# Performance work log

Measured on AMD Instinct MI355X. Metric: run time of the kernel, lower is better.

## Reference

```python
import jax, jax.numpy as jnp
import numpy as np


def _pn_layer(x, W):
    # x: [B, d]; W: [N, d+1, d+1]. z = [x, 1]; out[b, n] = z_b^T W_n z_b
    z = jnp.concatenate([x, jnp.ones((x.shape[0], 1), dtype=x.dtype)], axis=1)  # [B, d+1]
    zW = jnp.einsum('bi,nij->bnj', z, W)      # [B, N, d+1]
    return jnp.einsum('bnj,bj->bn', zW, z)    # [B, N]


def setup_inputs() -> dict:
    key = jax.random.key(0)
    k_x, k1, k2, k3, kw, kb = jax.random.split(key, 6)
    B, D = 2048, 256
    return {
        'x': jax.random.normal(k_x, (B, D), dtype=jnp.float32),
        'W1': jax.random.normal(k1, (256, D + 1, D + 1), dtype=jnp.float32),
        'W2': jax.random.normal(k2, (256, 257, 257), dtype=jnp.float32),
        'W3': jax.random.normal(k3, (256, 257, 257), dtype=jnp.float32),
        'w_out': jax.random.normal(kw, (1, 256), dtype=jnp.float32),
        'b_out': jax.random.normal(kb, (1,), dtype=jnp.float32),
    }


def reference(x, W1, W2, W3, w_out, b_out):
    h = _pn_layer(x, W1)   # [B, 256]
    h = _pn_layer(h, W2)   # [B, 256]
    h = _pn_layer(h, W3)   # [B, 256]
    return h @ w_out.T + b_out  # [B, 1]
```

## Files before the change

### kernel.cpp

```cpp
#include <hip/hip_runtime.h>
#include <hip/hip_bf16.h>

typedef __attribute__((ext_vector_type(8))) short short8;
typedef __attribute__((ext_vector_type(4))) float f32x4;

#define DDIM 256
#define WROW 257
#define WSTRIDE 66049
#define WT3_N 36864

__device__ __forceinline__ unsigned short f2bf(float f) {
    unsigned int u = __float_as_uint(f);
    u += 0x7fff + ((u >> 16) & 1);
    return (unsigned short)(u >> 16);
}
__device__ __forceinline__ float bf2f(unsigned short s) {
    return __uint_as_float(((unsigned int)s) << 16);
}


__global__ __launch_bounds__(256) void conv_w3_kernel(
    const float* __restrict__ Wf, unsigned short* __restrict__ Wt3,
    float* __restrict__ Vt, float* __restrict__ Dv)
{
    __shared__ float tKJ[64][65];
    __shared__ float tJK[64][65];
    const int TJ[10] = {0,1,1,2,2,2,3,3,3,3};
    const int TK[10] = {0,0,1,0,1,2,0,1,2,3};
    const int tid = threadIdx.x;
    const int n   = blockIdx.y;
    const int tj  = TJ[blockIdx.x];
    const int tk  = TK[blockIdx.x];
    const float* Wn = Wf + (size_t)n * WSTRIDE;
    if (blockIdx.x == 0) {
        int j = tid;
        Vt[n * 256 + j] = Wn[(size_t)j * WROW + 256] + Wn[65792 + j];
        if (j == 0) Dv[n] = Wn[66048];
    }
    #pragma unroll
    for (int it = 0; it < 4; ++it) {
        int idx = it * 256 + tid;
        int r   = idx >> 4;
        int c4  = (idx & 15) * 4;
        float4 vKJ = *reinterpret_cast<const float4*>(&Wn[(size_t)(tk * 64 + r) * WROW + tj * 64 + c4]);
        float4 vJK = *reinterpret_cast<const float4*>(&Wn[(size_t)(tj * 64 + r) * WROW + tk * 64 + c4]);
        tKJ[r][c4 + 0] = vKJ.x; tKJ[r][c4 + 1] = vKJ.y; tKJ[r][c4 + 2] = vKJ.z; tKJ[r][c4 + 3] = vKJ.w;
        tJK[r][c4 + 0] = vJK.x; tJK[r][c4 + 1] = vJK.y; tJK[r][c4 + 2] = vJK.z; tJK[r][c4 + 3] = vJK.w;
    }
    __syncthreads();
    unsigned short* out = Wt3 + (size_t)n * WT3_N;
    #pragma unroll
    for (int it = 0; it < 8; ++it) {
        int jl = it * 8 + (tid >> 5);
        int k2 = (tid & 31) * 2;
        int jg = tj * 64 + jl;
        int kg = tk * 64 + k2;
        int jt = jg >> 5;
        int kk = kg >> 5;
        if (kk <= jt) {
            float sc = (kk == jt) ? 0.5f : 1.0f;
            float v0 = sc * (tKJ[k2][jl]     + tJK[jl][k2]);
            float v1 = sc * (tKJ[k2 + 1][jl] + tJK[jl][k2 + 1]);
            unsigned int u = (unsigned)f2bf(v0) | ((unsigned)f2bf(v1) << 16);
            int half = (jg >> 4) & 1;
            int r15l = jg & 15;
            int qwl  = (kg >> 3) & 3;
            int kr   = kg & 7;
            size_t sidx = (size_t)(jt * (jt + 1) / 2 + kk) * 1024 + half * 512
                        + (qwl * 16 + r15l) * 8 + kr;
            *reinterpret_cast<unsigned int*>(out + sidx) = u;
        }
    }
}

__device__ __forceinline__ void xe_gather3(const unsigned short* T, unsigned short* Xe2,
                                           int bx, int tid) {
    const int lane = tid & 63, g = tid >> 6, qw = (tid >> 4) & 3, r15 = tid & 15;
    #pragma unroll
    for (int it = 0; it < 16; ++it) {
        int c  = g * 16 + it;
        int h  = c >> 5;
        int jt = (c >> 2) & 7;
        int m  = c & 3;
        int rbase = h * 64 + m * 16 + qw * 4;
        int jA = jt * 32 + r15;
        unsigned int u0 = T[(rbase + 0) * 256 + jA];
        unsigned int u1 = T[(rbase + 1) * 256 + jA];
        unsigned int u2 = T[(rbase + 2) * 256 + jA];
        unsigned int u3 = T[(rbase + 3) * 256 + jA];
        unsigned int v0 = T[(rbase + 0) * 256 + jA + 16];
        unsigned int v1 = T[(rbase + 1) * 256 + jA + 16];
        unsigned int v2 = T[(rbase + 2) * 256 + jA + 16];
        unsigned int v3 = T[(rbase + 3) * 256 + jA + 16];
        uint4 w = make_uint4(u0 | (u1 << 16), u2 | (u3 << 16),
                             v0 | (v1 << 16), v2 | (v3 << 16));
        *reinterpret_cast<uint4*>(Xe2 + ((size_t)(bx * 2 + h) * 16384 + jt * 2048 + m * 512 + lane * 8)) = w;
    }
}

__global__ __launch_bounds__(256) void conv_x_rm_kernel(
    const float* __restrict__ X, unsigned short* __restrict__ Xbf, unsigned short* __restrict__ Xe2)
{
    __shared__ __align__(16) unsigned short T[128 * 256];
    const int tid = threadIdx.x;
    const int b0 = blockIdx.x * 128;
    const float4* Xv = reinterpret_cast<const float4*>(X + (size_t)b0 * 256);
    uint2* Xo = reinterpret_cast<uint2*>(Xbf + (size_t)b0 * 256);
    #pragma unroll
    for (int it = 0; it < 32; ++it) {
        int idx4 = it * 256 + tid;
        float4 v = Xv[idx4];
        uint2 p;
        p.x = (unsigned)f2bf(v.x) | ((unsigned)f2bf(v.y) << 16);
        p.y = (unsigned)f2bf(v.z) | ((unsigned)f2bf(v.w) << 16);
        *reinterpret_cast<uint2*>(&T[idx4 * 4]) = p;
        Xo[idx4] = p;
    }
    __syncthreads();
    xe_gather3(T, Xe2, blockIdx.x, tid);
}

__global__ __launch_bounds__(256) void conv_x_tr_kernel(
    const unsigned short* __restrict__ Hsrc, unsigned short* __restrict__ Xbf,
    unsigned short* __restrict__ Xe2)
{
    __shared__ __align__(16) unsigned short T[128 * 256];
    const int tid = threadIdx.x;
    const int b0 = blockIdx.x * 128;
    #pragma unroll
    for (int it = 0; it < 64; ++it) {
        int lin = it * 256 + tid;
        int k = lin >> 6, bp = lin & 63;
        unsigned int v = *reinterpret_cast<const unsigned int*>(Hsrc + (size_t)k * 2048 + b0 + bp * 2);
        T[(bp * 2) * 256 + k]     = (unsigned short)(v & 0xffff);
        T[(bp * 2 + 1) * 256 + k] = (unsigned short)(v >> 16);
    }
    __syncthreads();
    uint4* Xo = reinterpret_cast<uint4*>(Xbf + (size_t)b0 * 256);
    #pragma unroll
    for (int it = 0; it < 16; ++it) {
        int idx8 = it * 256 + tid;
        Xo[idx8] = *reinterpret_cast<uint4*>(&T[idx8 * 8]);
    }
    xe_gather3(T, Xe2, blockIdx.x, tid);
}

__global__ __launch_bounds__(256, 2) void pn10_kernel(
    const unsigned short* __restrict__ Xbf,
    const unsigned short* __restrict__ Xe2,
    const unsigned short* __restrict__ Wt3,
    const float* __restrict__ Vt,
    const float* __restrict__ Dv,
    unsigned short* __restrict__ Ht)
{
    __shared__ __align__(16) char Xl[32768];

    const int tid  = threadIdx.x;
    const int lane = tid & 63;
    const int wv   = tid >> 6;
    const int qw   = lane >> 4;
    const int r15  = lane & 15;

    const int fid = blockIdx.y * 32 + blockIdx.x;
    const int bt  = (fid >> 3) & 31;
    const int ng  = (fid & 7) + ((fid >> 8) << 3);
    const int n   = ng * 4 + wv;
    const int b0  = bt * 64;

    {
        const uint4* xs = reinterpret_cast<const uint4*>(Xbf + (size_t)b0 * 256);
        #pragma unroll
        for (int c = 0; c < 8; ++c) {
            int idx = c * 256 + tid;
            uint4 v = xs[idx];
            int L = idx * 16;
            int d = L ^ (((L >> 9) & 7) << 4);
            *reinterpret_cast<uint4*>(&Xl[d]) = v;
        }
    }

    const unsigned short* wp = Wt3 + (size_t)n * WT3_N + (size_t)lane * 8;
    const float* vn = Vt + n * 256;
    const unsigned short* xe = Xe2 + (size_t)bt * 16384 + (size_t)lane * 8;

    short8 bA0 = *reinterpret_cast<const short8*>(wp);
    short8 bB0 = *reinterpret_cast<const short8*>(wp + 512);
    short8 bA1 = *reinterpret_cast<const short8*>(wp + 1024);
    short8 bB1 = *reinterpret_cast<const short8*>(wp + 1024 + 512);
    short8 bA2 = *reinterpret_cast<const short8*>(wp + 2048);
    short8 bB2 = *reinterpret_cast<const short8*>(wp + 2048 + 512);
    short8 bA3 = *reinterpret_cast<const short8*>(wp + 3072);
    short8 bB3 = *reinterpret_cast<const short8*>(wp + 3072 + 512);

    short8 e0 = *reinterpret_cast<const short8*>(xe);
    short8 e1 = *reinterpret_cast<const short8*>(xe + 512);
    short8 e2 = *reinterpret_cast<const short8*>(xe + 1024);
    short8 e3 = *reinterpret_cast<const short8*>(xe + 1536);
    float vA = vn[r15], vB = vn[16 + r15];

    float ps[4][4];
    f32x4 a0[4], a1[4];
    #pragma unroll
    for (int m = 0; m < 4; ++m) {
        a0[m] = f32x4{0.f, 0.f, 0.f, 0.f};
        a1[m] = f32x4{0.f, 0.f, 0.f, 0.f};
        #pragma unroll
        for (int r = 0; r < 4; ++r) ps[m][r] = 0.f;
    }

    int jt = 0, kk = 0;
    int slab_pf = 4;

    __syncthreads();

    auto body = [&](short8& bA, short8& bB) {
        #pragma unroll
        for (int m = 0; m < 4; ++m) {
            const int row = m * 16 + r15;
            const int byte = (row * 512 + kk * 64 + qw * 16) ^ ((row & 7) << 4);
            short8 a = *reinterpret_cast<const short8*>(&Xl[byte]);
            a0[m] = __builtin_amdgcn_mfma_f32_16x16x32_bf16(a, bA, a0[m], 0, 0, 0);
            a1[m] = __builtin_amdgcn_mfma_f32_16x16x32_bf16(a, bB, a1[m], 0, 0, 0);
        }
        if (kk == jt) {
            #pragma unroll
            for (int r = 0; r < 4; ++r) {
                ps[0][r] += (a0[0][r] + vA) * bf2f((unsigned short)e0[r]) + (a1[0][r] + vB) * bf2f((unsigned short)e0[4 + r]);
                ps[1][r] += (a0[1][r] + vA) * bf2f((unsigned short)e1[r]) + (a1[1][r] + vB) * bf2f((unsigned short)e1[4 + r]);
                ps[2][r] += (a0[2][r] + vA) * bf2f((unsigned short)e2[r]) + (a1[2][r] + vB) * bf2f((unsigned short)e2[4 + r]);
                ps[3][r] += (a0[3][r] + vA) * bf2f((unsigned short)e3[r]) + (a1[3][r] + vB) * bf2f((unsigned short)e3[4 + r]);
            }
            #pragma unroll
            for (int m = 0; m < 4; ++m) {
                a0[m] = f32x4{0.f, 0.f, 0.f, 0.f};
                a1[m] = f32x4{0.f, 0.f, 0.f, 0.f};
            }
            jt += 1; kk = 0;
            const int jc = (jt < 8) ? jt : 7;
            e0 = *reinterpret_cast<const short8*>(xe + jc * 2048);
            e1 = *reinterpret_cast<const short8*>(xe + jc * 2048 + 512);
            e2 = *reinterpret_cast<const short8*>(xe + jc * 2048 + 1024);
            e3 = *reinterpret_cast<const short8*>(xe + jc * 2048 + 1536);
            vA = vn[jc * 32 + r15];
            vB = vn[jc * 32 + 16 + r15];
        } else {
            kk += 1;
        }
        const int sc = (slab_pf <= 35) ? slab_pf : 35;
        const unsigned short* pf = wp + (size_t)sc * 1024;
        bA = *reinterpret_cast<const short8*>(pf);
        bB = *reinterpret_cast<const short8*>(pf + 512);
        slab_pf += 1;
    };

    #pragma unroll 1
    for (int i = 0; i < 9; ++i) {
        body(bA0, bB0);
        body(bA1, bB1);
        body(bA2, bB2);
        body(bA3, bB3);
    }

    #pragma unroll
    for (int off = 1; off <= 8; off <<= 1)
        #pragma unroll
        for (int m = 0; m < 4; ++m)
            #pragma unroll
            for (int r = 0; r < 4; ++r) ps[m][r] += __shfl_xor(ps[m][r], off, 64);

    if (r15 == 0) {
        const float dn = Dv[n];
        #pragma unroll
        for (int m = 0; m < 4; ++m)
            #pragma unroll
            for (int r = 0; r < 4; ++r)
                Ht[(size_t)n * 2048 + b0 + m * 16 + qw * 4 + r] = f2bf(ps[m][r] + dn);
    }
}

__global__ __launch_bounds__(256) void out_tr_kernel(
    const unsigned short* __restrict__ H3, const float* __restrict__ w_out,
    const float* __restrict__ b_out, float* __restrict__ out)
{
    __shared__ float red2[256];
    const int tid = threadIdx.x;
    const int b = blockIdx.x * 128 + (tid & 127);
    const int half = tid >> 7;
    float s = 0.f;
    #pragma unroll 8
    for (int k = 0; k < 128; ++k) {
        int nn = half * 128 + k;
        s += bf2f(H3[(size_t)nn * 2048 + b]) * w_out[nn];
    }
    red2[tid] = s;
    __syncthreads();
    if (tid < 128) out[b] = red2[tid] + red2[tid + 128] + b_out[0];
}


__global__ __launch_bounds__(256, 2) void pn_layer_kernel(
    const float* __restrict__ X, const float* __restrict__ W, float* __restrict__ H)
{
    __shared__ __align__(16) char Xl[64 * 256 * 2];
    __shared__ __align__(16) char Wl[2][256 * 32 * 2];
    const int tid  = threadIdx.x;
    const int lane = tid & 63;
    const int wv   = tid >> 6;
    const int qw   = lane >> 4;
    const int r15  = lane & 15;
    const int n  = blockIdx.y;
    const int b0 = blockIdx.x * 64;
    const float* Wn = W + (size_t)n * WSTRIDE;
    {
        const float4* Xv = reinterpret_cast<const float4*>(X + (size_t)b0 * DDIM);
        #pragma unroll
        for (int it = 0; it < 16; ++it) {
            int idx4 = tid + it * 256;
            int r = idx4 >> 6, c4 = idx4 & 63;
            float4 v = Xv[r * 64 + c4];
            uint2 p;
            p.x = (unsigned)f2bf(v.x) | ((unsigned)f2bf(v.y) << 16);
            p.y = (unsigned)f2bf(v.z) | ((unsigned)f2bf(v.w) << 16);
            int byte = (r * 512 + c4 * 8) ^ ((r & 7) << 4);
            *reinterpret_cast<uint2*>(&Xl[byte]) = p;
        }
    }
    f32x4 acc[4][4];
    #pragma unroll
    for (int nf = 0; nf < 4; ++nf) {
        int j = wv * 64 + nf * 16 + r15;
        float vj = Wn[(size_t)j * WROW + 256] + Wn[65792 + j];
        #pragma unroll
        for (int m = 0; m < 4; ++m) acc[m][nf] = f32x4{vj, vj, vj, vj};
    }
    auto stageW = [&](int buf, int kk) {
        const int k0 = kk * 32;
        const int j  = tid;
        float t[32];
        #pragma unroll
        for (int k = 0; k < 32; ++k) t[k] = Wn[(size_t)(k0 + k) * WROW + j];
        char* Wb = Wl[buf];
        #pragma unroll
        for (int g = 0; g < 4; ++g) {
            unsigned int p0 = (unsigned)f2bf(t[g*8+0]) | ((unsigned)f2bf(t[g*8+1]) << 16);
            unsigned int p1 = (unsigned)f2bf(t[g*8+2]) | ((unsigned)f2bf(t[g*8+3]) << 16);
            unsigned int p2 = (unsigned)f2bf(t[g*8+4]) | ((unsigned)f2bf(t[g*8+5]) << 16);
            unsigned int p3 = (unsigned)f2bf(t[g*8+6]) | ((unsigned)f2bf(t[g*8+7]) << 16);
            int byte = (j * 64 + g * 16) ^ ((j & 7) << 4);
            *reinterpret_cast<uint4*>(&Wb[byte]) = make_uint4(p0, p1, p2, p3);
        }
    };
    auto computeK = [&](int buf, int kk) {
        char* Wb = Wl[buf];
        short8 a[4], bbf[4];
        #pragma unroll
        for (int m = 0; m < 4; ++m) {
            int row = m * 16 + r15;
            int byte = (row * 512 + kk * 64 + qw * 16) ^ ((row & 7) << 4);
            a[m] = *reinterpret_cast<short8*>(&Xl[byte]);
        }
        #pragma unroll
        for (int nf = 0; nf < 4; ++nf) {
            int j = wv * 64 + nf * 16 + r15;
            int byte = (j * 64 + qw * 16) ^ ((j & 7) << 4);
            bbf[nf] = *reinterpret_cast<short8*>(&Wb[byte]);
        }
        #pragma unroll
        for (int m = 0; m < 4; ++m)
            #pragma unroll
            for (int nf = 0; nf < 4; ++nf)
                acc[m][nf] = __builtin_amdgcn_mfma_f32_16x16x32_bf16(a[m], bbf[nf], acc[m][nf], 0, 0, 0);
    };
    stageW(0, 0);
    int cur = 0;
    #pragma unroll
    for (int kk = 0; kk < 8; ++kk) {
        __syncthreads();
        if (kk < 7) stageW(cur ^ 1, kk + 1);
        computeK(cur, kk);
        cur ^= 1;
    }
    float ps[16];
    #pragma unroll
    for (int i = 0; i < 16; ++i) ps[i] = 0.f;
    #pragma unroll
    for (int m = 0; m < 4; ++m)
        #pragma unroll
        for (int nf = 0; nf < 4; ++nf) {
            int j = wv * 64 + nf * 16 + r15;
            #pragma unroll
            for (int r = 0; r < 4; ++r) {
                int brow = m * 16 + qw * 4 + r;
                int byte = (brow * 512 + j * 2) ^ ((brow & 7) << 4);
                float xv = bf2f(*reinterpret_cast<unsigned short*>(&Xl[byte]));
                ps[m * 4 + r] += acc[m][nf][r] * xv;
            }
        }
    #pragma unroll
    for (int off = 1; off <= 8; off <<= 1)
        #pragma unroll
        for (int i = 0; i < 16; ++i) ps[i] += __shfl_xor(ps[i], off, 64);
    __syncthreads();
    float* red = reinterpret_cast<float*>(Wl);
    if (r15 == 0) {
        #pragma unroll
        for (int m = 0; m < 4; ++m)
            #pragma unroll
            for (int r = 0; r < 4; ++r)
                red[wv * 64 + m * 16 + qw * 4 + r] = ps[m * 4 + r];
    }
    __syncthreads();
    if (tid < 64) {
        float s = red[tid] + red[64 + tid] + red[128 + tid] + red[192 + tid] + Wn[66048];
        H[(size_t)(b0 + tid) * DDIM + n] = s;
    }
}

__global__ __launch_bounds__(256) void out_kernel(
    const float* __restrict__ H, const float* __restrict__ w_out,
    const float* __restrict__ b_out, float* __restrict__ out)
{
    int b = blockIdx.x * 4 + (threadIdx.x >> 6);
    int lane = threadIdx.x & 63;
    const float* h = H + (size_t)b * 256;
    float s = 0.f;
    #pragma unroll
    for (int c = 0; c < 4; ++c) s += h[lane + c * 64] * w_out[lane + c * 64];
    #pragma unroll
    for (int off = 1; off < 64; off <<= 1) s += __shfl_xor(s, off, 64);
    if (lane == 0) out[b] = s + b_out[0];
}

extern "C" void kernel_launch(void* const* d_in, const int* in_sizes, int n_in,
                              void* d_out, int out_size, void* d_ws, size_t ws_size,
                              hipStream_t stream) {
    const float* x    = (const float*)d_in[0];
    const float* W1   = (const float*)d_in[1];
    const float* W2   = (const float*)d_in[2];
    const float* W3   = (const float*)d_in[3];
    const float* wout = (const float*)d_in[4];
    const float* bout = (const float*)d_in[5];
    float* out = (float*)d_out;

    const size_t WT3_BYTES = (size_t)256 * WT3_N * 2;
    const size_t XB_BYTES  = (size_t)2048 * 256 * 2;
    const size_t XE2_BYTES = (size_t)32 * 16384 * 2;
    const size_t VT_BYTES  = 256 * 256 * 4;
    const size_t DV_BYTES  = 1024;
    const size_t HT_BYTES  = (size_t)256 * 2048 * 2;
    const size_t need = WT3_BYTES + XB_BYTES + XE2_BYTES + VT_BYTES + DV_BYTES + HT_BYTES;

    dim3 blk(256, 1, 1);

    if (ws_size >= need) {
        char* p = (char*)d_ws;
        unsigned short* Wt3 = (unsigned short*)p;              p += WT3_BYTES;
        unsigned short* Xbf = (unsigned short*)p;              p += XB_BYTES;
        unsigned short* Xe2 = (unsigned short*)p;              p += XE2_BYTES;
        float*          Vt  = (float*)p;                       p += VT_BYTES;
        float*          Dv  = (float*)p;                       p += DV_BYTES;
        unsigned short* Ht  = (unsigned short*)p;

        const float* Ws[3] = {W1, W2, W3};

        dim3 wgrid(10, 256), lgrid(32, 64), xgrid(16);
        for (int L = 0; L < 3; ++L) {
            if (L == 0) conv_x_rm_kernel<<<xgrid, blk, 0, stream>>>(x, Xbf, Xe2);
            else        conv_x_tr_kernel<<<xgrid, blk, 0, stream>>>(Ht, Xbf, Xe2);
            conv_w3_kernel<<<wgrid, blk, 0, stream>>>(Ws[L], Wt3, Vt, Dv);
            pn10_kernel<<<lgrid, blk, 0, stream>>>(Xbf, Xe2, Wt3, Vt, Dv, Ht);
        }
        out_tr_kernel<<<xgrid, blk, 0, stream>>>(Ht, wout, bout, out);
    } else {
        float* h1 = (float*)d_ws;
        float* h2 = h1 + 2048 * 256;
        dim3 grid(32, 256);
        pn_layer_kernel<<<grid, blk, 0, stream>>>(x,  W1, h1);
        pn_layer_kernel<<<grid, blk, 0, stream>>>(h1, W2, h2);
        pn_layer_kernel<<<grid, blk, 0, stream>>>(h2, W3, h1);
        out_kernel<<<512, blk, 0, stream>>>(h1, wout, bout, out);
    }
}
```

Measured before the change: 270.8 us.

## Vectorize packed-weight store in conv kernel and raise pn10 occupancy bound

The weight conversion kernel now assigns whole 16x32 packed chunks to each wavefront, so every lane writes a single 16-byte uint4 instead of scattered 4-byte stores, and only the chunks in the lower-triangular region are enumerated. This reduces the number of store instructions and improves write coalescing. The main pn10 kernel's launch bound is raised from 2 to 3 blocks per SM, which caps register use to allow more resident blocks and risks register spills.

```diff
diff --git a/kernel.cpp b/kernel.cpp
--- a/kernel.cpp
+++ b/kernel.cpp
@@ -48,28 +48,33 @@
         tJK[r][c4 + 0] = vJK.x; tJK[r][c4 + 1] = vJK.y; tJK[r][c4 + 2] = vJK.z; tJK[r][c4 + 3] = vJK.w;
     }
     __syncthreads();
+    const int wv = tid >> 6, lane = tid & 63;
     unsigned short* out = Wt3 + (size_t)n * WT3_N;
-    #pragma unroll
-    for (int it = 0; it < 8; ++it) {
-        int jl = it * 8 + (tid >> 5);
-        int k2 = (tid & 31) * 2;
-        int jg = tj * 64 + jl;
-        int kg = tk * 64 + k2;
-        int jt = jg >> 5;
-        int kk = kg >> 5;
-        if (kk <= jt) {
-            float sc = (kk == jt) ? 0.5f : 1.0f;
-            float v0 = sc * (tKJ[k2][jl]     + tJK[jl][k2]);
-            float v1 = sc * (tKJ[k2 + 1][jl] + tJK[jl][k2 + 1]);
-            unsigned int u = (unsigned)f2bf(v0) | ((unsigned)f2bf(v1) << 16);
-            int half = (jg >> 4) & 1;
-            int r15l = jg & 15;
-            int qwl  = (kg >> 3) & 3;
-            int kr   = kg & 7;
-            size_t sidx = (size_t)(jt * (jt + 1) / 2 + kk) * 1024 + half * 512
-                        + (qwl * 16 + r15l) * 8 + kr;
-            *reinterpret_cast<unsigned int*>(out + sidx) = u;
-        }
+    int ch[8]; int nch = 0;
+    #pragma unroll
+    for (int jtl = 0; jtl < 2; ++jtl)
+        #pragma unroll
+        for (int kkl = 0; kkl < 2; ++kkl) {
+            if (tk * 2 + kkl <= tj * 2 + jtl) {
+                ch[nch++] = jtl * 4 + kkl * 2 + 0;
+                ch[nch++] = jtl * 4 + kkl * 2 + 1;
+            }
+        }
+    for (int c = wv; c < nch; c += 4) {
+        const int jtl = ch[c] >> 2, kkl = (ch[c] >> 1) & 1, half = ch[c] & 1;
+        const int jtg = tj * 2 + jtl, kkg = tk * 2 + kkl;
+        const float sc = (kkg == jtg) ? 0.5f : 1.0f;
+        const int jl = jtl * 32 + half * 16 + (lane & 15);
+        const int k0 = kkl * 32 + (lane >> 4) * 8;
+        unsigned int w[4];
+        #pragma unroll
+        for (int t = 0; t < 4; ++t) {
+            float lo = sc * (tKJ[k0 + 2 * t][jl]     + tJK[jl][k0 + 2 * t]);
+            float hi = sc * (tKJ[k0 + 2 * t + 1][jl] + tJK[jl][k0 + 2 * t + 1]);
+            w[t] = (unsigned)f2bf(lo) | ((unsigned)f2bf(hi) << 16);
+        }
+        size_t sidx = (size_t)(jtg * (jtg + 1) / 2 + kkg) * 1024 + half * 512 + lane * 8;
+        *reinterpret_cast<uint4*>(out + sidx) = make_uint4(w[0], w[1], w[2], w[3]);
     }
 }
 
@@ -145,7 +150,7 @@
     xe_gather3(T, Xe2, blockIdx.x, tid);
 }
 
-__global__ __launch_bounds__(256, 2) void pn10_kernel(
+__global__ __launch_bounds__(256, 3) void pn10_kernel(
     const unsigned short* __restrict__ Xbf,
     const unsigned short* __restrict__ Xe2,
     const unsigned short* __restrict__ Wt3,
```

Measured after the change: 272.7 us. About the same (+0.7%).
